# Performance work log

Measured on AMD Instinct MI355X. Metric: run time of the kernel, lower is better.

The kernel has to match this reference:

```python
import jax, jax.numpy as jnp
import numpy as np

HIDDEN = 4096
N_HEADS = 32
N_KV_HEADS = 8
HEAD_DIM = HIDDEN // N_HEADS  # 128
N_KV_GROUPS = N_HEADS // N_KV_HEADS  # 4
SEQ = 2048
BSZ = 1
ROPE_THETA = 10000.0


def _rope_cos_sin(seqlen, head_dim, dtype):
    # freqs_cis = polar(1, outer(t, theta^{-2i/d})) -> cos/sin tables [S, hd/2]
    inv_freq = 1.0 / (ROPE_THETA ** (jnp.arange(0, head_dim, 2, dtype=jnp.float32) / head_dim))
    t = jnp.arange(seqlen, dtype=jnp.float32)
    freqs = jnp.outer(t, inv_freq)  # [S, hd/2]
    return jnp.cos(freqs).astype(dtype), jnp.sin(freqs).astype(dtype)


def _apply_rotary(x, cos, sin):
    # x: [B, S, H, hd]. Torch code pairs (x[:hd/2], x[hd/2:]) as (real, imag):
    # out = concat(x1*cos - x2*sin, x1*sin + x2*cos)
    half = x.shape[-1] // 2
    x1, x2 = x[..., :half], x[..., half:]
    c = cos[None, :, None, :]  # [1, S, 1, hd/2]
    s = sin[None, :, None, :]
    return jnp.concatenate([x1 * c - x2 * s, x1 * s + x2 * c], axis=-1)


def setup_inputs() -> dict:
    key = jax.random.key(0)
    k1, k2, k3 = jax.random.split(key, 3)
    hidden_states = jax.random.normal(k1, (BSZ, SEQ, HIDDEN), dtype=jnp.float32)
    w_qkv = jax.random.normal(k2, (HIDDEN, (N_HEADS + 2 * N_KV_HEADS) * HEAD_DIM), dtype=jnp.float32) * 0.02
    w_o = jax.random.normal(k3, (HIDDEN, HIDDEN), dtype=jnp.float32) * 0.02
    # HF-style additive causal mask [1, 1, S, S]
    causal = jnp.tril(jnp.ones((SEQ, SEQ), dtype=bool))
    attention_mask = jnp.where(causal, 0.0, -1e9).astype(jnp.float32)[None, None]
    return {"hidden_states": hidden_states, "w_qkv": w_qkv, "w_o": w_o,
            "attention_mask": attention_mask}


def reference(hidden_states, w_qkv, w_o, attention_mask):
    bsz, seqlen, _ = hidden_states.shape
    # fused (dequantized) QKV projection
    xqkv = jnp.einsum('bsh,hd->bsd', hidden_states, w_qkv)
    xqkv = xqkv.reshape(bsz, seqlen, N_HEADS + 2 * N_KV_HEADS, HEAD_DIM)
    xq = xqkv[:, :, :N_HEADS]                      # [B, S, 32, 128]
    xk = xqkv[:, :, N_HEADS:N_HEADS + N_KV_HEADS]  # [B, S, 8, 128]
    xv = xqkv[:, :, -N_KV_HEADS:]                  # [B, S, 8, 128]

    cos, sin = _rope_cos_sin(seqlen, HEAD_DIM, hidden_states.dtype)
    xq = _apply_rotary(xq, cos, sin)
    xk = _apply_rotary(xk, cos, sin)

    # GQA: repeat_interleave kv heads along head dim
    keys = jnp.repeat(xk, N_KV_GROUPS, axis=2)    # [B, S, 32, 128]
    values = jnp.repeat(xv, N_KV_GROUPS, axis=2)

    q = xq.transpose(0, 2, 1, 3)   # [B, H, S, D]
    k = keys.transpose(0, 2, 1, 3)
    v = values.transpose(0, 2, 1, 3)

    scores = jnp.einsum('bhqd,bhkd->bhqk', q, k) / np.sqrt(HEAD_DIM)
    scores = scores + attention_mask
    probs = jax.nn.softmax(scores.astype(jnp.float32), axis=-1).astype(q.dtype)
    out = jnp.einsum('bhqk,bhkd->bhqd', probs, v)
    attention_weight = out.transpose(0, 2, 1, 3).reshape(bsz, seqlen, -1)
    attn_output = jnp.einsum('bsh,ho->bso', attention_weight, w_o)
    return attn_output
```

## Files before the change

kernel.cpp:

```cpp
#include <hip/hip_runtime.h>
#include <stdint.h>

typedef unsigned short u16;
typedef __bf16 bf8 __attribute__((ext_vector_type(8)));
typedef float f32x4 __attribute__((ext_vector_type(4)));

#define SEQ 2048
#define HIDDEN 4096
#define DQKV 6144
#define HD 128

#define GLOAD_LDS16(g, l)                                                            \
    __builtin_amdgcn_global_load_lds((const __attribute__((address_space(1))) void*)(g), \
                                     (__attribute__((address_space(3))) void*)(l), 16, 0, 0)

__device__ __forceinline__ u16 f2bf(float f) {
    union { float f; unsigned u; } v{f};
    unsigned r = (v.u + 0x7fff + ((v.u >> 16) & 1)) >> 16;
    return (u16)r;
}
__device__ __forceinline__ float bf2f(u16 b) {
    union { unsigned u; float f; } v;
    v.u = ((unsigned)b) << 16;
    return v.f;
}


__global__ void convert_bf16_kernel(const float* __restrict__ in, u16* __restrict__ out) {
    int i = (blockIdx.x * 256 + threadIdx.x) * 4;
    float4 v = *(const float4*)(in + i);
    u16 o[4] = {f2bf(v.x), f2bf(v.y), f2bf(v.z), f2bf(v.w)};
    *(uint2*)(out + i) = *(uint2*)o;
}

__global__ void transpose_w_kernel(const float* __restrict__ in, u16* __restrict__ out, int K, int N) {
    __shared__ u16 tile[64][65];
    int tn = N >> 6;
    int bk = blockIdx.x / tn, bn = blockIdx.x % tn;
    int k0 = bk * 64, n0 = bn * 64;
    int c = threadIdx.x & 63, r0 = threadIdx.x >> 6;
#pragma unroll
    for (int r = r0; r < 64; r += 4)
        tile[r][c] = f2bf(in[(size_t)(k0 + r) * N + n0 + c]);
    __syncthreads();
#pragma unroll
    for (int r = r0; r < 64; r += 4)
        out[(size_t)(n0 + r) * K + k0 + c] = tile[c][r];
}

__global__ void rope_kernel(u16* __restrict__ x) {
    const int row = blockIdx.x / 10, hg = blockIdx.x % 10;
    const int head = hg * 4 + (threadIdx.x >> 6), j = threadIdx.x & 63;
    u16* p = x + (size_t)row * DQKV + head * HD + j;
    float x1 = bf2f(p[0]), x2 = bf2f(p[64]);
    float inv = exp2f(-(float)j * 0.20762050593045952f);
    float s, c;
    sincosf((float)row * inv, &s, &c);
    p[0] = f2bf(x1 * c - x2 * s);
    p[64] = f2bf(x1 * s + x2 * c);
}

__global__ void transpose_v_kernel(const u16* __restrict__ xqkv, u16* __restrict__ vt) {
    __shared__ u16 tile[64][65];
    int h = blockIdx.x >> 6;
    int t = blockIdx.x & 63;
    int s0 = (t >> 1) * 64, d0 = (t & 1) * 64;
    int c = threadIdx.x & 63, r0 = threadIdx.x >> 6;
    const u16* src = xqkv + (40 + h) * HD + d0;
#pragma unroll
    for (int r = r0; r < 64; r += 4)
        tile[r][c] = src[(size_t)(s0 + r) * DQKV + c];
    __syncthreads();
    u16* dst = vt + ((size_t)h * HD + d0) * SEQ + s0;
#pragma unroll
    for (int r = r0; r < 64; r += 4)
        dst[(size_t)r * SEQ + c] = tile[c][r];
}

template <int BM, int BN, int MODE>
__global__ __launch_bounds__(512, 2) void gemm8p_kernel(const u16* __restrict__ A,
                                                        const u16* __restrict__ BT,
                                                        u16* __restrict__ Cbf,
                                                        float* __restrict__ Cf) {
    constexpr int WAVES_N = (MODE == 0) ? 2 : 4;
    constexpr int WM = BM * WAVES_N / 128;
    constexpr int WN = BN / (WAVES_N * 16);
    constexpr int MP = WM / 4;
    static_assert(WM >= 4 && MP >= 1, "wave split arithmetic");
    constexpr int NLA = BM / 64, NLB = BN / 64, NL = NLA + NLB;
    constexpr int NBN = ((MODE == 0) ? DQKV : HIDDEN) / BN;
    constexpr int NBM = SEQ / BM;
    constexpr int CSTR = (MODE == 0) ? DQKV : HIDDEN;
    constexpr int NT = 64;
    static_assert(NBM * NBN == 256, "grid must be exactly 256 blocks");
    __shared__ __align__(16) u16 lds[2][(BM + BN) * 64];

    const int tid = threadIdx.x;
    const int w = tid >> 6, l = tid & 63, l15 = l & 15, q4 = l >> 4;
    const int wm = w / WAVES_N, wn = w % WAVES_N;

    const int xcd = blockIdx.x & 7, wi = blockIdx.x >> 3;
    int bm, bn;
    if constexpr (NBN == 32) {
        bm = (xcd >> 2) * 4 + (wi >> 3);
        bn = (xcd & 3) * 8 + (wi & 7);
    } else {
        bm = (xcd & 3) * 4 + (wi >> 3);
        bn = (xcd >> 2) * 8 + (wi & 7);
    }

    const int srow = tid >> 3;
    const int scol = ((tid & 7) ^ ((tid >> 3) & 7)) << 4;
    const char* spA[NLA];
    const char* spB[NLB];
#pragma unroll
    for (int L = 0; L < NLA; ++L)
        spA[L] = (const char*)(A + (size_t)(bm * BM + L * 64 + srow) * 4096) + scol;
#pragma unroll
    for (int L = 0; L < NLB; ++L)
        spB[L] = (const char*)(BT + (size_t)(bn * BN + L * 64 + srow) * 4096) + scol;

#define STG_A(L, tt, b) GLOAD_LDS16(spA[L] + (size_t)(tt) * 128, &lds[b][(L) * 4096 + w * 512])
#define STG_B(L, tt, b) GLOAD_LDS16(spB[L] + (size_t)(tt) * 128, &lds[b][BM * 64 + (L) * 4096 + w * 512])

#pragma unroll
    for (int L = 0; L < NLA; ++L) STG_A(L, 0, 0);
#pragma unroll
    for (int L = 0; L < NLB; ++L) STG_B(L, 0, 0);
#pragma unroll
    for (int L = 0; L < NLA; ++L) STG_A(L, 1, 1);
#pragma unroll
    for (int L = 0; L < NLB; ++L) STG_B(L, 1, 1);
    if constexpr (NL == 7) asm volatile("s_waitcnt vmcnt(7)" ::: "memory");
    else                   asm volatile("s_waitcnt vmcnt(6)" ::: "memory");
    asm volatile("s_barrier" ::: "memory");

    const int c0x = (q4 * 16) ^ ((l15 & 7) << 4);
    const int c1x = c0x ^ 64;

    f32x4 acc[WM][WN] = {};
    bf8 breg[WN][2];

#pragma unroll 1
    for (int t = 0; t < NT; ++t) {
        const int cur = t & 1;
        const char* ldsA = (const char*)&lds[cur][0];
        const char* ldsB = ldsA + BM * 128;
#pragma unroll
        for (int p = 0; p < 4; ++p) {
            if (p == 1 && t < NT - 2) {
#pragma unroll
                for (int L = 0; L < NLB; ++L) STG_B(L, t + 2, cur);
            }
            bf8 areg[MP][2];
#pragma unroll
            for (int j = 0; j < MP; ++j) {
                const char* rp = ldsA + (wm * (WM * 16) + (p * MP + j) * 16 + l15) * 128;
                areg[j][0] = *(const bf8*)(rp + c0x);
                areg[j][1] = *(const bf8*)(rp + c1x);
            }
            if (p == 0) {
#pragma unroll
                for (int nf = 0; nf < WN; ++nf) {
                    const char* rp = ldsB + (wn * (WN * 16) + nf * 16 + l15) * 128;
                    breg[nf][0] = *(const bf8*)(rp + c0x);
                    breg[nf][1] = *(const bf8*)(rp + c1x);
                }
            }
            asm volatile("s_barrier" ::: "memory");
            asm volatile("s_waitcnt lgkmcnt(0)" ::: "memory");
            __builtin_amdgcn_s_setprio(1);
#pragma unroll
            for (int j = 0; j < MP; ++j)
#pragma unroll
                for (int nf = 0; nf < WN; ++nf)
#pragma unroll
                    for (int ks = 0; ks < 2; ++ks)
                        acc[p * MP + j][nf] = __builtin_amdgcn_mfma_f32_16x16x32_bf16(
                            areg[j][ks], breg[nf][ks], acc[p * MP + j][nf], 0, 0, 0);
            __builtin_amdgcn_s_setprio(0);
            asm volatile("s_barrier" ::: "memory");
        }
        if (t < NT - 2) {
#pragma unroll
            for (int L = 0; L < NLA; ++L) STG_A(L, t + 2, cur);
            if constexpr (NL == 7) asm volatile("s_waitcnt vmcnt(7)" ::: "memory");
            else                   asm volatile("s_waitcnt vmcnt(6)" ::: "memory");
        } else if (t == NT - 2) {
            asm volatile("s_waitcnt vmcnt(0)" ::: "memory");
        }
        asm volatile("s_barrier" ::: "memory");
    }
#undef STG_A
#undef STG_B

    const int rowb = bm * BM + wm * (WM * 16);
    const int colb = bn * BN + wn * (WN * 16);
#pragma unroll
    for (int mf = 0; mf < WM; ++mf)
#pragma unroll
        for (int nf = 0; nf < WN; ++nf)
#pragma unroll
            for (int r = 0; r < 4; ++r) {
                const int row = rowb + mf * 16 + q4 * 4 + r;
                const int col = colb + nf * 16 + l15;
                if constexpr (MODE == 0)
                    Cbf[(size_t)row * CSTR + col] = f2bf(acc[mf][nf][r]);
                else
                    Cf[(size_t)row * CSTR + col] = acc[mf][nf][r];
            }
}

#define PSTR 72
__global__ __launch_bounds__(256) void attn_kernel(const u16* __restrict__ xqkv,
                                                   const u16* __restrict__ vt,
                                                   u16* __restrict__ aw) {
    __shared__ __align__(16) u16 sm[16384 + 128 * PSTR];
    const int tid = threadIdx.x, w = tid >> 6, l = tid & 63, l15 = l & 15, q4 = l >> 4;
    const int qh = blockIdx.x & 31;
    const int qslot = blockIdx.x >> 5;
    const int qt = (qslot < 8) ? qslot : 23 - qslot;
    const int kh = qh >> 2;

    {
        const u16* gq = xqkv + (size_t)(qt * 128 + (l >> 2)) * DQKV + qh * HD + w * 32 + (l & 3) * 8;
#pragma unroll
        for (int i = 0; i < 8; ++i)
            GLOAD_LDS16(gq + (size_t)i * 16 * DQKV, &sm[w * 4096 + i * 512]);
    }
    __syncthreads();
    bf8 qf[4][2];
#pragma unroll
    for (int ks = 0; ks < 4; ++ks)
#pragma unroll
        for (int mt = 0; mt < 2; ++mt)
            qf[ks][mt] = *(const bf8*)&sm[ks * 4096 + (w * 32 + mt * 16 + l15) * 32 + q4 * 8];
    __syncthreads();

    f32x4 O[2][8] = {};
    float plrow[2][4] = {};

    u16* ldsK = sm;
    u16* ldsV = sm + 8192;
    u16* ldsP = sm + 16384;
    const int nkt = 2 * qt + 2;
    const float cs = 0.12751744f;

    const int sr8 = l >> 3;
    const int sc8 = (l & 7) ^ sr8;
    const u16* gk_base = xqkv + (size_t)((w >> 1) * 32 + sr8) * DQKV + (32 + kh) * HD + (w & 1) * 64 + sc8 * 8;
    u16* ldsK_dst = ldsK + (w & 1) * 4096 + (w >> 1) * 2048;
    const u16* gv_base = vt + ((size_t)kh * HD + w * 32 + sr8) * SEQ + sc8 * 8;
    u16* ldsV_dst = ldsV + w * 2048;

    const int cswz = (q4 ^ (l15 & 7)) << 4;
    const char* Kb = (const char*)ldsK;
    const char* Vb = (const char*)ldsV;

    for (int kt = 0; kt < nkt; ++kt) {
        {
            const u16* gk = gk_base + (size_t)(kt * 64) * DQKV;
#pragma unroll
            for (int i = 0; i < 4; ++i)
                GLOAD_LDS16(gk + (size_t)i * 8 * DQKV, ldsK_dst + i * 512);
        }
        {
            const u16* gv = gv_base + kt * 64;
#pragma unroll
            for (int i = 0; i < 4; ++i)
                GLOAD_LDS16(gv + (size_t)i * 8 * SEQ, ldsV_dst + i * 512);
        }
        __syncthreads();

        f32x4 S[2][4] = {};
#pragma unroll
        for (int ks = 0; ks < 4; ++ks) {
            bf8 kf[4];
#pragma unroll
            for (int nt = 0; nt < 4; ++nt)
                kf[nt] = *(const bf8*)(Kb + (ks >> 1) * 8192 + (nt * 16 + l15) * 128
                                       + (cswz ^ ((ks & 1) << 6)));
#pragma unroll
            for (int mt = 0; mt < 2; ++mt)
#pragma unroll
                for (int nt = 0; nt < 4; ++nt)
                    S[mt][nt] = __builtin_amdgcn_mfma_f32_16x16x32_bf16(qf[ks][mt], kf[nt], S[mt][nt], 0, 0, 0);
        }

        const bool domask = (kt >= 2 * qt);
#pragma unroll
        for (int mt = 0; mt < 2; ++mt)
#pragma unroll
            for (int r = 0; r < 4; ++r) {
                const int row = qt * 128 + w * 32 + mt * 16 + q4 * 4 + r;
#pragma unroll
                for (int nt = 0; nt < 4; ++nt) {
                    float t = S[mt][nt][r] * cs;
                    if (domask && (kt * 64 + nt * 16 + l15 > row)) t = -1e30f;
                    float p = exp2f(t);
                    plrow[mt][r] += p;
                    ldsP[(w * 32 + mt * 16 + q4 * 4 + r) * PSTR + nt * 16 + l15] = f2bf(p);
                }
            }

#pragma unroll
        for (int pk = 0; pk < 2; ++pk) {
            bf8 pf[2], vf[8];
#pragma unroll
            for (int mt = 0; mt < 2; ++mt)
                pf[mt] = *(const bf8*)&ldsP[(w * 32 + mt * 16 + l15) * PSTR + pk * 32 + q4 * 8];
#pragma unroll
            for (int nt = 0; nt < 8; ++nt)
                vf[nt] = *(const bf8*)(Vb + (nt * 16 + l15) * 128 + (cswz ^ (pk << 6)));
#pragma unroll
            for (int mt = 0; mt < 2; ++mt)
#pragma unroll
                for (int nt = 0; nt < 8; ++nt)
                    O[mt][nt] = __builtin_amdgcn_mfma_f32_16x16x32_bf16(pf[mt], vf[nt], O[mt][nt], 0, 0, 0);
        }
        __syncthreads();
    }

#pragma unroll
    for (int mt = 0; mt < 2; ++mt)
#pragma unroll
        for (int r = 0; r < 4; ++r) {
            float ls = plrow[mt][r];
#pragma unroll
            for (int off = 1; off <= 8; off <<= 1)
                ls += __shfl_xor(ls, off, 64);
            const float linv = 1.0f / ls;
            const int row = qt * 128 + w * 32 + mt * 16 + q4 * 4 + r;
#pragma unroll
            for (int nt = 0; nt < 8; ++nt)
                aw[(size_t)row * 4096 + qh * HD + nt * 16 + l15] = f2bf(O[mt][nt][r] * linv);
        }
}


extern "C" void kernel_launch(void* const* d_in, const int* in_sizes, int n_in,
                              void* d_out, int out_size, void* d_ws, size_t ws_size,
                              hipStream_t stream) {
    const float* hs = (const float*)d_in[0];
    const float* wqkv = (const float*)d_in[1];
    const float* wo = (const float*)d_in[2];
    float* out = (float*)d_out;

    char* ws = (char*)d_ws;
    const size_t oHbf = 0;
    const size_t oWqkvT = oHbf + (size_t)SEQ * HIDDEN * 2;
    const size_t oWoT = oWqkvT + (size_t)DQKV * HIDDEN * 2;
    const size_t oXQKV = oWoT + (size_t)HIDDEN * HIDDEN * 2;
    const size_t oVT = oXQKV + (size_t)SEQ * DQKV * 2;
    const size_t oAW = oVT + (size_t)8 * HD * SEQ * 2;
    const size_t total = oAW + (size_t)SEQ * HIDDEN * 2;
    if (ws_size < total) return;

    u16* Hbf = (u16*)(ws + oHbf);
    u16* WqkvT = (u16*)(ws + oWqkvT);
    u16* WoT = (u16*)(ws + oWoT);
    u16* XQKV = (u16*)(ws + oXQKV);
    u16* VT = (u16*)(ws + oVT);
    u16* AW = (u16*)(ws + oAW);

    convert_bf16_kernel<<<(SEQ * HIDDEN) / 1024, 256, 0, stream>>>(hs, Hbf);
    transpose_w_kernel<<<(HIDDEN / 64) * (DQKV / 64), 256, 0, stream>>>(wqkv, WqkvT, HIDDEN, DQKV);
    transpose_w_kernel<<<(HIDDEN / 64) * (HIDDEN / 64), 256, 0, stream>>>(wo, WoT, HIDDEN, HIDDEN);
    gemm8p_kernel<256, 192, 0><<<256, 512, 0, stream>>>(Hbf, WqkvT, XQKV, nullptr);
    rope_kernel<<<SEQ * 10, 256, 0, stream>>>(XQKV);
    transpose_v_kernel<<<8 * 64, 256, 0, stream>>>(XQKV, VT);
    attn_kernel<<<512, 256, 0, stream>>>(XQKV, VT, AW);
    gemm8p_kernel<128, 256, 1><<<256, 512, 0, stream>>>(AW, WoT, nullptr, out);
}
```

Baseline: 524.7 us.

## Merge prep and rope/V-transpose launches; retile QKV GEMM waves and split A prefetch

Merges three prep kernels (hidden-state bf16 conversion and two weight transposes) into one launch, and merges rope with the V transpose into another. Merging is safe because rope writes only Q/K columns while the transpose reads only V columns. The QKV GEMM (MODE 0) now uses a 2x4 wave layout (WM=8, WN=3) instead of 4x2. It also issues half of its next-tile A global-to-LDS loads mid-iteration (phase 2) rather than all at the end, to spread memory traffic. This trades more A-fragment LDS reads per wave for fewer B reads and removes launch gaps; the retiling changes register pressure and LDS access balance.

```diff
diff --git a/kernel.cpp b/kernel.cpp
--- a/kernel.cpp
+++ b/kernel.cpp
@@ -25,20 +25,31 @@
     return v.f;
 }
 
-
-__global__ void convert_bf16_kernel(const float* __restrict__ in, u16* __restrict__ out) {
-    int i = (blockIdx.x * 256 + threadIdx.x) * 4;
-    float4 v = *(const float4*)(in + i);
-    u16 o[4] = {f2bf(v.x), f2bf(v.y), f2bf(v.z), f2bf(v.w)};
-    *(uint2*)(out + i) = *(uint2*)o;
-}
-
-__global__ void transpose_w_kernel(const float* __restrict__ in, u16* __restrict__ out, int K, int N) {
+__global__ void prep_kernel(const float* __restrict__ hs,
+                            const float* __restrict__ wqkv,
+                            const float* __restrict__ wo,
+                            u16* __restrict__ Hbf,
+                            u16* __restrict__ WqkvT,
+                            u16* __restrict__ WoT) {
     __shared__ u16 tile[64][65];
-    int tn = N >> 6;
-    int bk = blockIdx.x / tn, bn = blockIdx.x % tn;
-    int k0 = bk * 64, n0 = bn * 64;
-    int c = threadIdx.x & 63, r0 = threadIdx.x >> 6;
+    int b = blockIdx.x;
+    const int tid = threadIdx.x;
+    if (b < 8192) {
+        int i = (b * 256 + tid) * 4;
+        float4 v = *(const float4*)(hs + i);
+        u16 o[4] = {f2bf(v.x), f2bf(v.y), f2bf(v.z), f2bf(v.w)};
+        *(uint2*)(Hbf + i) = *(uint2*)o;
+        return;
+    }
+    const float* in;
+    u16* out;
+    int K, N;
+    if (b < 14336) { b -= 8192;  in = wqkv; out = WqkvT; K = HIDDEN; N = DQKV; }
+    else           { b -= 14336; in = wo;   out = WoT;   K = HIDDEN; N = HIDDEN; }
+    const int tn = N >> 6;
+    const int bk = b / tn, bn = b % tn;
+    const int k0 = bk * 64, n0 = bn * 64;
+    const int c = tid & 63, r0 = tid >> 6;
 #pragma unroll
     for (int r = r0; r < 64; r += 4)
         tile[r][c] = f2bf(in[(size_t)(k0 + r) * N + n0 + c]);
@@ -48,25 +59,28 @@
         out[(size_t)(n0 + r) * K + k0 + c] = tile[c][r];
 }
 
-__global__ void rope_kernel(u16* __restrict__ x) {
-    const int row = blockIdx.x / 10, hg = blockIdx.x % 10;
-    const int head = hg * 4 + (threadIdx.x >> 6), j = threadIdx.x & 63;
-    u16* p = x + (size_t)row * DQKV + head * HD + j;
-    float x1 = bf2f(p[0]), x2 = bf2f(p[64]);
-    float inv = exp2f(-(float)j * 0.20762050593045952f);
-    float s, c;
-    sincosf((float)row * inv, &s, &c);
-    p[0] = f2bf(x1 * c - x2 * s);
-    p[64] = f2bf(x1 * s + x2 * c);
-}
-
-__global__ void transpose_v_kernel(const u16* __restrict__ xqkv, u16* __restrict__ vt) {
+__global__ void rope_tv_kernel(u16* __restrict__ x, u16* __restrict__ vt) {
     __shared__ u16 tile[64][65];
-    int h = blockIdx.x >> 6;
-    int t = blockIdx.x & 63;
-    int s0 = (t >> 1) * 64, d0 = (t & 1) * 64;
-    int c = threadIdx.x & 63, r0 = threadIdx.x >> 6;
-    const u16* src = xqkv + (40 + h) * HD + d0;
+    int b = blockIdx.x;
+    const int tid = threadIdx.x;
+    if (b < 20480) {
+        const int row = b / 10, hg = b % 10;
+        const int head = hg * 4 + (tid >> 6), j = tid & 63;
+        u16* p = x + (size_t)row * DQKV + head * HD + j;
+        float x1 = bf2f(p[0]), x2 = bf2f(p[64]);
+        float inv = exp2f(-(float)j * 0.20762050593045952f);
+        float s, c;
+        sincosf((float)row * inv, &s, &c);
+        p[0] = f2bf(x1 * c - x2 * s);
+        p[64] = f2bf(x1 * s + x2 * c);
+        return;
+    }
+    b -= 20480;
+    const int h = b >> 6;
+    const int t = b & 63;
+    const int s0 = (t >> 1) * 64, d0 = (t & 1) * 64;
+    const int c = tid & 63, r0 = tid >> 6;
+    const u16* src = x + (40 + h) * HD + d0;
 #pragma unroll
     for (int r = r0; r < 64; r += 4)
         tile[r][c] = src[(size_t)(s0 + r) * DQKV + c];
@@ -82,11 +96,9 @@
                                                         const u16* __restrict__ BT,
                                                         u16* __restrict__ Cbf,
                                                         float* __restrict__ Cf) {
-    constexpr int WAVES_N = (MODE == 0) ? 2 : 4;
-    constexpr int WM = BM * WAVES_N / 128;
-    constexpr int WN = BN / (WAVES_N * 16);
+    constexpr int WM = BM / 32;
+    constexpr int WN = BN / 64;
     constexpr int MP = WM / 4;
-    static_assert(WM >= 4 && MP >= 1, "wave split arithmetic");
     constexpr int NLA = BM / 64, NLB = BN / 64, NL = NLA + NLB;
     constexpr int NBN = ((MODE == 0) ? DQKV : HIDDEN) / BN;
     constexpr int NBM = SEQ / BM;
@@ -97,7 +109,7 @@
 
     const int tid = threadIdx.x;
     const int w = tid >> 6, l = tid & 63, l15 = l & 15, q4 = l >> 4;
-    const int wm = w / WAVES_N, wn = w % WAVES_N;
+    const int wm = w >> 2, wn = w & 3;
 
     const int xcd = blockIdx.x & 7, wi = blockIdx.x >> 3;
     int bm, bn;
@@ -152,10 +164,16 @@
 #pragma unroll
                 for (int L = 0; L < NLB; ++L) STG_B(L, t + 2, cur);
             }
+            if constexpr (BM == 256) {
+                if (p == 2 && t < NT - 2) {
+                    STG_A(0, t + 2, cur);
+                    STG_A(2, t + 2, cur);
+                }
+            }
             bf8 areg[MP][2];
 #pragma unroll
             for (int j = 0; j < MP; ++j) {
-                const char* rp = ldsA + (wm * (WM * 16) + (p * MP + j) * 16 + l15) * 128;
+                const char* rp = ldsA + (wm * (BM / 2) + (p * MP + j) * 16 + l15) * 128;
                 areg[j][0] = *(const bf8*)(rp + c0x);
                 areg[j][1] = *(const bf8*)(rp + c1x);
             }
@@ -182,8 +200,8 @@
             asm volatile("s_barrier" ::: "memory");
         }
         if (t < NT - 2) {
-#pragma unroll
-            for (int L = 0; L < NLA; ++L) STG_A(L, t + 2, cur);
+            if constexpr (BM == 256) { STG_A(1, t + 2, cur); STG_A(3, t + 2, cur); }
+            else                     { STG_A(0, t + 2, cur); STG_A(1, t + 2, cur); }
             if constexpr (NL == 7) asm volatile("s_waitcnt vmcnt(7)" ::: "memory");
             else                   asm volatile("s_waitcnt vmcnt(6)" ::: "memory");
         } else if (t == NT - 2) {
@@ -194,7 +212,7 @@
 #undef STG_A
 #undef STG_B
 
-    const int rowb = bm * BM + wm * (WM * 16);
+    const int rowb = bm * BM + wm * (BM / 2);
     const int colb = bn * BN + wn * (WN * 16);
 #pragma unroll
     for (int mf = 0; mf < WM; ++mf)
@@ -363,12 +381,9 @@
     u16* VT = (u16*)(ws + oVT);
     u16* AW = (u16*)(ws + oAW);
 
-    convert_bf16_kernel<<<(SEQ * HIDDEN) / 1024, 256, 0, stream>>>(hs, Hbf);
-    transpose_w_kernel<<<(HIDDEN / 64) * (DQKV / 64), 256, 0, stream>>>(wqkv, WqkvT, HIDDEN, DQKV);
-    transpose_w_kernel<<<(HIDDEN / 64) * (HIDDEN / 64), 256, 0, stream>>>(wo, WoT, HIDDEN, HIDDEN);
+    prep_kernel<<<18432, 256, 0, stream>>>(hs, wqkv, wo, Hbf, WqkvT, WoT);
     gemm8p_kernel<256, 192, 0><<<256, 512, 0, stream>>>(Hbf, WqkvT, XQKV, nullptr);
-    rope_kernel<<<SEQ * 10, 256, 0, stream>>>(XQKV);
-    transpose_v_kernel<<<8 * 64, 256, 0, stream>>>(XQKV, VT);
+    rope_tv_kernel<<<20992, 256, 0, stream>>>(XQKV, VT);
     attn_kernel<<<512, 256, 0, stream>>>(XQKV, VT, AW);
     gemm8p_kernel<128, 256, 1><<<256, 512, 0, stream>>>(AW, WoT, nullptr, out);
 }
```

Result: faster. 508.9 us (-3.0%).
